# Performance work log

Hardware: AMD Instinct MI355X
Metric: run time of the kernel (lower is better)

Reference implementation:

```python
import jax, jax.numpy as jnp
import numpy as np

N_F = 100000   # station (feature) nodes
N_H = 49152    # healpix nodes (12*4^6)
E = 400000     # edges per timestep
T_IN = 12
T_OUT = 12
H = 64         # hidden_size (must equal 64: cat with Linear(1,64) output)
A_H = 2 * H    # AttentionReadout hidden_size


def setup_inputs() -> dict:
    key = jax.random.key(0)
    ks = jax.random.split(key, 20)
    feat = jax.random.normal(ks[0], (N_F, T_IN, 1), dtype=jnp.float32)
    enc_src = jax.random.randint(ks[1], (E,), 0, N_F, dtype=jnp.int32)
    enc_dst = jax.random.randint(ks[2], (E,), 0, N_H, dtype=jnp.int32)
    dec_src = jax.random.randint(ks[3], (E,), 0, N_H, dtype=jnp.int32)
    dec_dst = jax.random.randint(ks[4], (E,), 0, N_F, dtype=jnp.int32)
    s = 0.05
    return {
        'feat': feat,
        'enc_src': enc_src, 'enc_dst': enc_dst,
        'dec_src': dec_src, 'dec_dst': dec_dst,
        # per-timestep encoder GraphConv(1 -> H) weights
        'W_enc': jax.random.normal(ks[5], (T_IN, 1, H), jnp.float32) * s,
        'b_enc': jnp.zeros((T_IN, H), jnp.float32),
        # MLP processor over time: Linear(T_IN -> T_OUT) + ReLU
        'W_proc': jax.random.normal(ks[6], (T_IN, T_OUT), jnp.float32) * s,
        'b_proc': jnp.zeros((T_OUT,), jnp.float32),
        # per-timestep decoder GraphConv(H -> H)
        'W_dec': jax.random.normal(ks[7], (T_OUT, H, H), jnp.float32) * s,
        'b_dec': jnp.zeros((T_OUT, H), jnp.float32),
        # decoder self.linears = Linear(1, 64)
        'W_lin': jax.random.normal(ks[8], (1, H), jnp.float32) * s,
        'b_lin': jnp.zeros((H,), jnp.float32),
        # AttentionReadout: score MLP (H -> 2H -> 1), output proj (H -> 1)
        'W_a1': jax.random.normal(ks[9], (H, A_H), jnp.float32) * s,
        'b_a1': jnp.zeros((A_H,), jnp.float32),
        'W_a2': jax.random.normal(ks[10], (A_H, 1), jnp.float32) * s,
        'b_a2': jnp.zeros((1,), jnp.float32),
        'W_o': jax.random.normal(ks[11], (H, 1), jnp.float32) * s,
        'b_o': jnp.zeros((1,), jnp.float32),
    }


def _gcn_norms(src, dst, n_src, n_dst):
    # DGL GraphConv norm='both': deg clamped to min 1, ^-0.5
    ones = jnp.ones(src.shape[0], jnp.float32)
    out_deg = jnp.maximum(jax.ops.segment_sum(ones, src, num_segments=n_src), 1.0)
    in_deg = jnp.maximum(jax.ops.segment_sum(ones, dst, num_segments=n_dst), 1.0)
    return out_deg ** -0.5, in_deg ** -0.5


def reference(feat, enc_src, enc_dst, dec_src, dec_dst,
              W_enc, b_enc, W_proc, b_proc, W_dec, b_dec,
              W_lin, b_lin, W_a1, b_a1, W_a2, b_a2, W_o, b_o):
    c_se, c_de = _gcn_norms(enc_src, enc_dst, N_F, N_H)
    c_sd, c_dd = _gcn_norms(dec_src, dec_dst, N_H, N_F)

    # ---- Graph_Encoder: per-t GraphConv(station -> healpix), 1 -> H ----
    x = jnp.nan_to_num(feat)                                  # [N_f, T_in, 1]
    msg = x * c_se[:, None, None]
    agg = jax.ops.segment_sum(msg[enc_src], enc_dst, num_segments=N_H)  # [N_h, T_in, 1]
    h_enc = jax.nn.leaky_relu(
        jnp.einsum('nti,tih->nth', agg * c_de[:, None, None], W_enc) + b_enc)  # [N_h, T_in, H]

    # ---- MLP_Processor: Linear over the time axis, T_in -> T_out, ReLU ----
    h_proc = jax.nn.relu(jnp.einsum('nth,to->noh', h_enc, W_proc)
                         + b_proc[:, None])                    # [N_h, T_out, H]
    h_proc_t = jnp.swapaxes(h_proc, 0, 1)                      # [T_out, N_h, H]

    # ---- Graph_Decoder: per-t GraphConv(healpix -> station) + Linear(prev) + AttentionReadout ----
    def step(y_prev, inp):
        h_t, W_t, b_t = inp                                    # h_t: [N_h, H]
        m = h_t * c_sd[:, None]
        a = jax.ops.segment_sum(m[dec_src], dec_dst, num_segments=N_F)  # [N_f, H]
        space1 = jax.nn.leaky_relu((a * c_dd[:, None]) @ W_t + b_t)     # [N_f, H]
        space2 = y_prev @ W_lin + b_lin                                 # [N_f, H]
        stacked = jnp.stack([space1, space2], axis=0)                   # [2, N_f, H]
        scores = jnp.tanh(stacked @ W_a1 + b_a1) @ W_a2 + b_a2          # [2, N_f, 1]
        alpha = jax.nn.softmax(scores, axis=0)
        states = jnp.sum(alpha * stacked, axis=0)                       # [N_f, H]
        y = states @ W_o + b_o                                          # [N_f, 1]
        return y, y

    y0 = x[:, -1]                                              # t{input_length-1}
    _, ys = jax.lax.scan(step, y0, (h_proc_t, W_dec, b_dec))
    return ys                                                  # [T_out, N_f, 1]
```

## Files before the change

kernel.cpp:

```cpp
#include <hip/hip_runtime.h>
#include <hip/hip_bf16.h>
#include <hip/hip_fp16.h>

#define NF 100000
#define NH 49152
#define EDG 400000
#define SLOTD 24
#define SLOTE 32

typedef __attribute__((ext_vector_type(8))) short short8;
typedef __attribute__((ext_vector_type(4))) float float4v;
typedef unsigned short u16;
typedef unsigned int u32;

__device__ __forceinline__ u16 f2b(float x) {
    u32 u = __float_as_uint(x);
    u32 r = u + 0x7FFFu + ((u >> 16) & 1u);
    return (u16)(r >> 16);
}
__device__ __forceinline__ u32 cvt_pk(float lo, float hi) {
    u32 r;
    asm("v_cvt_pk_bf16_f32 %0, %1, %2" : "=v"(r) : "v"(lo), "v"(hi));
    return r;
}
__device__ __forceinline__ __half2 h2(u32 v) { union { u32 u; __half2 h; } c; c.u = v; return c.h; }
__device__ __forceinline__ float fast_tanh(float x) {
    float t = __builtin_amdgcn_exp2f(x * 2.885390081777927f);
    return fmaf(-2.0f, __builtin_amdgcn_rcpf(t + 1.0f), 1.0f);
}

#define PN1 (NF * 12)
#define PN3 298304
#define PN4 384
#define PREB 5856
__global__ void init_all(u32* __restrict__ csrD32,
                         u32* __restrict__ degcnt, u32* __restrict__ mzero, int zstride,
                         const float* __restrict__ W_dec, const float* __restrict__ W_a1,
                         u16* __restrict__ fragWdec, u16* __restrict__ fragWa1,
                         const float* __restrict__ W_lin, const float* __restrict__ b_lin,
                         const float* __restrict__ b_a1, const float* __restrict__ W_o,
                         float* __restrict__ uvs, const float* __restrict__ W_a2,
                         float* __restrict__ gtab) {
    __shared__ float uvl[256];
    const int b = blockIdx.x;
    if (b < PREB) {
        int i = b * 256 + threadIdx.x;
        if (i < PN1) csrD32[i] = ((u32)NH << 16) | (u32)NH;
        else if (i < PN1 + PN3) degcnt[i - PN1] = 0u;
        else if (i < PN1 + PN3 + PN4) {
            int j = i - PN1 - PN3;
            mzero[(j >> 7) * (size_t)zstride + (j & 127)] = 0u;
        }
    } else if (b < PREB + 28) {
        int gid = (b - PREB) * 256 + threadIdx.x;
        if (gid >= 7168) return;
        int L = gid & 63;
        int f = gid >> 6;
        int q = L >> 4, cb = L & 15;
        if (f < 96) {
            int fr = f & 7;
            int c = fr >> 1, kc = fr & 1;
            int k0 = kc * 32 + q * 8;
            int nn = c * 16 + cb;
            int t = f >> 3;
            #pragma unroll
            for (int j = 0; j < 8; ++j)
                fragWdec[(f * 64 + L) * 8 + j] = f2b(W_dec[t * 4096 + (k0 + j) * 64 + nn]);
        } else {
            int fr = f - 96;
            int c2 = fr >> 1, kc = fr & 1;
            int k0 = kc * 32 + q * 8;
            int nn = c2 * 16 + cb;
            #pragma unroll
            for (int j = 0; j < 8; ++j)
                fragWa1[(fr * 64 + L) * 8 + j] = f2b(W_a1[(k0 + j) * 128 + nn]);
        }
    } else if (b == PREB + 28) {
        int k = threadIdx.x;
        if (k < 128) {
            float su = 0.f, sv = 0.f;
            for (int h = 0; h < 64; ++h) {
                su = fmaf(W_lin[h], W_a1[h * 128 + k], su);
                sv = fmaf(b_lin[h], W_a1[h * 128 + k], sv);
            }
            uvs[k] = su;
            uvs[128 + k] = sv + b_a1[k];
            if (k == 0) {
                float a = 0.f, bb = 0.f;
                for (int h = 0; h < 64; ++h) {
                    a = fmaf(W_lin[h], W_o[h], a);
                    bb = fmaf(b_lin[h], W_o[h], bb);
                }
                uvs[256] = a;
                uvs[257] = bb;
            }
        }
    } else {
        int k = threadIdx.x;
        if (k < 128) {
            float su = 0.f, sv = 0.f;
            for (int h = 0; h < 64; ++h) {
                su = fmaf(W_lin[h], W_a1[h * 128 + k], su);
                sv = fmaf(b_lin[h], W_a1[h * 128 + k], sv);
            }
            uvl[k] = su;
            uvl[128 + k] = sv + b_a1[k];
        }
        __syncthreads();
        int i = (b - PREB - 29) * 256 + threadIdx.x;
        if (i <= 16384) {
            float y = fmaf((float)i, 1.f / 256.f, -32.f);
            float s = 0.f;
            for (int kk = 0; kk < 128; ++kk)
                s = fmaf(fast_tanh(fmaf(y, uvl[kk], uvl[128 + kk])), W_a2[kk], s);
            gtab[i] = s;
        }
    }
}

__global__ void fill_slotted(const int* __restrict__ enc_src, const int* __restrict__ enc_dst,
                             const int* __restrict__ dec_src, const int* __restrict__ dec_dst,
                             int* __restrict__ cntD, u16* __restrict__ csrD, float* __restrict__ deg_sd,
                             int* __restrict__ cntE, u32* __restrict__ csrE, float* __restrict__ deg_se) {
    int e = blockIdx.x * 256 + threadIdx.x;
    if (e >= EDG) return;
    int ds = dec_src[e], dd = dec_dst[e];
    int i1 = atomicAdd(&cntD[dd], 1);
    if (i1 < SLOTD) csrD[(size_t)dd * SLOTD + i1] = (u16)ds;
    atomicAdd(&deg_sd[ds], 1.0f);
    int es = enc_src[e], ed = enc_dst[e];
    int i2 = atomicAdd(&cntE[ed], 1);
    if (i2 < SLOTE) csrE[(size_t)ed * SLOTE + i2] = (u32)es;
    atomicAdd(&deg_se[es], 1.0f);
}

__global__ __launch_bounds__(256) void enc_make(
    const float* __restrict__ feat, const float* __restrict__ deg_se,
    const int* __restrict__ cntE, const u32* __restrict__ csrE,
    const float* __restrict__ deg_sd, const float* __restrict__ W_enc,
    const float* __restrict__ b_enc, const float* __restrict__ W_proc,
    const float* __restrict__ b_proc, u16* __restrict__ m, size_t cstride) {
    __shared__ __align__(16) float aggl[4][12];
    const int tid = threadIdx.x, lane = tid & 63, wid = tid >> 6;
    const int n = blockIdx.x * 4 + wid;
    const int q = lane >> 2, l = lane & 3;
    int cntRaw = cntE[n];
    int cnt = cntRaw > SLOTE ? SLOTE : cntRaw;
    const u32* cp = csrE + (size_t)n * SLOTE;
    float4 a = {0.f, 0.f, 0.f, 0.f};
    if (l < 3) {
        for (int e = q; e < cnt; e += 16) {
            u32 s = cp[e];
            float c = rsqrtf(fmaxf(deg_se[s], 1.0f));
            float4 w = *(const float4*)(feat + (size_t)s * 12 + l * 4);
            w.x = (w.x != w.x) ? 0.f : w.x; w.y = (w.y != w.y) ? 0.f : w.y;
            w.z = (w.z != w.z) ? 0.f : w.z; w.w = (w.w != w.w) ? 0.f : w.w;
            a.x = fmaf(w.x, c, a.x); a.y = fmaf(w.y, c, a.y);
            a.z = fmaf(w.z, c, a.z); a.w = fmaf(w.w, c, a.w);
        }
    }
    #pragma unroll
    for (int mm = 4; mm < 64; mm <<= 1) {
        a.x += __shfl_xor(a.x, mm); a.y += __shfl_xor(a.y, mm);
        a.z += __shfl_xor(a.z, mm); a.w += __shfl_xor(a.w, mm);
    }
    if (q == 0 && l < 3) *(float4*)(&aggl[wid][l * 4]) = a;
    asm volatile("s_waitcnt lgkmcnt(0)" ::: "memory");

    const int h = lane;
    float cde = rsqrtf(fmaxf((float)cntRaw, 1.0f));
    float csd = rsqrtf(fmaxf(deg_sd[n], 1.0f));
    float he[12];
    #pragma unroll
    for (int ti = 0; ti < 12; ++ti) {
        float av = aggl[wid][ti] * cde;
        float x = fmaf(av, W_enc[ti * 64 + h], b_enc[ti * 64 + h]);
        he[ti] = x > 0.f ? x : 0.01f * x;
    }
    #pragma unroll
    for (int c = 0; c < 3; ++c) {
        float s0v[4];
        #pragma unroll
        for (int tt = 0; tt < 4; ++tt) {
            int t = c * 4 + tt;
            float s = b_proc[t];
            #pragma unroll
            for (int ti = 0; ti < 12; ++ti) s = fmaf(he[ti], W_proc[ti * 12 + t], s);
            s0v[tt] = fmaxf(s, 0.f) * csd;
        }
        u16 r0 = __half_as_ushort(__float2half(s0v[0]));
        u16 r1 = __half_as_ushort(__float2half(s0v[1]));
        u16 r2 = __half_as_ushort(__float2half(s0v[2]));
        u16 r3 = __half_as_ushort(__float2half(s0v[3]));
        u32 o0 = ((u32)r1 << 16) | r0;
        u32 o1 = ((u32)r3 << 16) | r2;
        u32* dst = (u32*)(m + c * cstride + (size_t)n * 256 + h * 4);
        dst[0] = o0; dst[1] = o1;
    }
}

__global__ __launch_bounds__(256) void enc_gather(const float* __restrict__ feat,
                                                  const float* __restrict__ deg_se,
                                                  const int* __restrict__ cntE,
                                                  const u32* __restrict__ csrE,
                                                  float* __restrict__ agg) {
    const int tid = threadIdx.x, lane = tid & 63, wid = tid >> 6;
    const int grp = lane >> 2, l = lane & 3;
    const int dst = blockIdx.x * 64 + wid * 16 + grp;
    int cnt = cntE[dst];
    if (cnt > SLOTE) cnt = SLOTE;
    const u32* cp = csrE + (size_t)dst * SLOTE;
    float4 a = {0.f, 0.f, 0.f, 0.f};
    if (l < 3) {
        for (int e = 0; e < cnt; ++e) {
            u32 s = cp[e];
            float c = rsqrtf(fmaxf(deg_se[s], 1.0f));
            float4 w = *(const float4*)(feat + (size_t)s * 12 + l * 4);
            w.x = (w.x != w.x) ? 0.f : w.x; w.y = (w.y != w.y) ? 0.f : w.y;
            w.z = (w.z != w.z) ? 0.f : w.z; w.w = (w.w != w.w) ? 0.f : w.w;
            a.x = fmaf(w.x, c, a.x); a.y = fmaf(w.y, c, a.y);
            a.z = fmaf(w.z, c, a.z); a.w = fmaf(w.w, c, a.w);
        }
    }
    *(float4*)(agg + (size_t)dst * 16 + l * 4) = a;
}

__global__ void make_chunk(const float* __restrict__ agg, const int* __restrict__ cntE,
                           const float* __restrict__ deg_sd, const float* __restrict__ W_enc,
                           const float* __restrict__ b_enc, const float* __restrict__ W_proc,
                           const float* __restrict__ b_proc, u16* __restrict__ m, int t0) {
    int gid = blockIdx.x * 256 + threadIdx.x;
    if (gid >= NH * 64) return;
    int n = gid >> 6, h = gid & 63;
    float cde = rsqrtf(fmaxf((float)cntE[n], 1.0f));
    float csd = rsqrtf(fmaxf(deg_sd[n], 1.0f));
    float he[12];
    #pragma unroll
    for (int ti = 0; ti < 12; ++ti) {
        float a = agg[n * 16 + ti] * cde;
        float x = fmaf(a, W_enc[ti * 64 + h], b_enc[ti * 64 + h]);
        he[ti] = x > 0.f ? x : 0.01f * x;
    }
    u16 r[4];
    #pragma unroll
    for (int tt = 0; tt < 4; ++tt) {
        int t = t0 + tt;
        float s = b_proc[t];
        #pragma unroll
        for (int ti = 0; ti < 12; ++ti) s = fmaf(he[ti], W_proc[ti * 12 + t], s);
        s = fmaxf(s, 0.f) * csd;
        r[tt] = __half_as_ushort(__float2half(s));
    }
    u32 o0 = ((u32)r[1] << 16) | r[0];
    u32 o1 = ((u32)r[3] << 16) | r[2];
    u32* dst = (u32*)(m + (size_t)n * 256 + h * 4);
    dst[0] = o0; dst[1] = o1;
}

__device__ __forceinline__ void acc4(__half2* a8, const u16* mrow, u32 lo, u32 hi) {
    int s0 = (int)(lo & 0xFFFF), s1 = (int)(lo >> 16);
    int s2 = (int)(hi & 0xFFFF), s3 = (int)(hi >> 16);
    const uint4* r0 = (const uint4*)(mrow + (size_t)s0 * 256);
    const uint4* r1 = (const uint4*)(mrow + (size_t)s1 * 256);
    const uint4* r2 = (const uint4*)(mrow + (size_t)s2 * 256);
    const uint4* r3 = (const uint4*)(mrow + (size_t)s3 * 256);
    uint4 A0 = r0[0], B0 = r0[1];
    uint4 A1 = r1[0], B1 = r1[1];
    uint4 A2 = r2[0], B2 = r2[1];
    uint4 A3 = r3[0], B3 = r3[1];
    a8[0] = __hadd2(a8[0], __hadd2(__hadd2(h2(A0.x), h2(A1.x)), __hadd2(h2(A2.x), h2(A3.x))));
    a8[1] = __hadd2(a8[1], __hadd2(__hadd2(h2(A0.y), h2(A1.y)), __hadd2(h2(A2.y), h2(A3.y))));
    a8[2] = __hadd2(a8[2], __hadd2(__hadd2(h2(A0.z), h2(A1.z)), __hadd2(h2(A2.z), h2(A3.z))));
    a8[3] = __hadd2(a8[3], __hadd2(__hadd2(h2(A0.w), h2(A1.w)), __hadd2(h2(A2.w), h2(A3.w))));
    a8[4] = __hadd2(a8[4], __hadd2(__hadd2(h2(B0.x), h2(B1.x)), __hadd2(h2(B2.x), h2(B3.x))));
    a8[5] = __hadd2(a8[5], __hadd2(__hadd2(h2(B0.y), h2(B1.y)), __hadd2(h2(B2.y), h2(B3.y))));
    a8[6] = __hadd2(a8[6], __hadd2(__hadd2(h2(B0.z), h2(B1.z)), __hadd2(h2(B2.z), h2(B3.z))));
    a8[7] = __hadd2(a8[7], __hadd2(__hadd2(h2(B0.w), h2(B1.w)), __hadd2(h2(B2.w), h2(B3.w))));
}

__global__ __launch_bounds__(256, 4) void dec_batch(
    const u16* __restrict__ mbase, const int* __restrict__ cntD, const u16* __restrict__ csrD,
    const u16* __restrict__ fragWdec, const u16* __restrict__ fragWa1,
    const float* __restrict__ b_dec, const float* __restrict__ b_a1,
    const float* __restrict__ W_a2, const float* __restrict__ W_o,
    float* __restrict__ S1, float* __restrict__ PW, int t0p, size_t mstride) {
    __shared__ __align__(16) u16 zs[18432];

    const u16* m = mbase + (size_t)blockIdx.y * mstride;
    const int t0 = t0p + blockIdx.y * 4;
    const int tid = threadIdx.x, lane = tid & 63, wid = tid >> 6;
    const int nw = blockIdx.x * 64 + wid * 16;
    const int g16 = lane >> 4, c16 = lane & 15;
    u16* zw0 = zs + wid * 4608;

    int cdw[4]; float cdd[4]; int nnv[4];
    uint4 qa[4];
    #pragma unroll
    for (int k = 0; k < 4; ++k) {
        int n = nw + g16 * 4 + k;
        bool v = (n < NF);
        nnv[k] = v ? n : 0;
        int cd = cntD[nnv[k]];
        cdd[k] = v ? rsqrtf(fmaxf((float)cd, 1.0f)) : 0.f;
        cdw[k] = v ? (cd > SLOTD ? SLOTD : cd) : 0;
        qa[k] = *(const uint4*)(csrD + (size_t)nnv[k] * SLOTD);
    }
    int cdmax = max(max(cdw[0], cdw[1]), max(cdw[2], cdw[3]));

    __half2 acc[4][8];
    #pragma unroll
    for (int k = 0; k < 4; ++k)
        #pragma unroll
        for (int i = 0; i < 8; ++i)
            acc[k][i] = __half2{__half(0.f), __half(0.f)};

    const u16* mrow = m + c16 * 16;
    #pragma unroll
    for (int k = 0; k < 4; ++k) if (cdw[k] > 0) acc4(acc[k], mrow, qa[k].x, qa[k].y);
    #pragma unroll
    for (int k = 0; k < 4; ++k) if (cdw[k] > 4) acc4(acc[k], mrow, qa[k].z, qa[k].w);
    if (__any(cdmax > 8)) {
        #pragma unroll
        for (int k = 0; k < 4; ++k) if (cdw[k] > 8) qa[k] = *(const uint4*)(csrD + (size_t)nnv[k] * SLOTD + 8);
        #pragma unroll
        for (int k = 0; k < 4; ++k) if (cdw[k] > 8) acc4(acc[k], mrow, qa[k].x, qa[k].y);
        #pragma unroll
        for (int k = 0; k < 4; ++k) if (cdw[k] > 12) acc4(acc[k], mrow, qa[k].z, qa[k].w);
        if (__any(cdmax > 16)) {
            #pragma unroll
            for (int k = 0; k < 4; ++k) if (cdw[k] > 16) qa[k] = *(const uint4*)(csrD + (size_t)nnv[k] * SLOTD + 16);
            #pragma unroll
            for (int k = 0; k < 4; ++k) if (cdw[k] > 16) acc4(acc[k], mrow, qa[k].x, qa[k].y);
            #pragma unroll
            for (int k = 0; k < 4; ++k) if (cdw[k] > 20) acc4(acc[k], mrow, qa[k].z, qa[k].w);
        }
    }

    #pragma unroll
    for (int k = 0; k < 4; ++k) {
        int j = g16 * 4 + k;
        float s = cdd[k];
        #pragma unroll
        for (int p = 0; p < 2; ++p) {
            float2 c0 = __half22float2(acc[k][0 * 2 + p]);
            float2 c1 = __half22float2(acc[k][1 * 2 + p]);
            float2 c2 = __half22float2(acc[k][2 * 2 + p]);
            float2 c3 = __half22float2(acc[k][3 * 2 + p]);
            u32 oA0 = cvt_pk(c0.x * s, c1.x * s);
            u32 oA1 = cvt_pk(c2.x * s, c3.x * s);
            u32 oB0 = cvt_pk(c0.y * s, c1.y * s);
            u32 oB1 = cvt_pk(c2.y * s, c3.y * s);
            u32* dA = (u32*)(zw0 + (2 * p) * 1152 + j * 72 + c16 * 4);
            u32* dB = (u32*)(zw0 + (2 * p + 1) * 1152 + j * 72 + c16 * 4);
            dA[0] = oA0; dA[1] = oA1;
            dB[0] = oB0; dB[1] = oB1;
        }
    }
    asm volatile("s_waitcnt lgkmcnt(0)" ::: "memory");

    float baw[8], waw[8], wov[4];
    #pragma unroll
    for (int c8 = 0; c8 < 8; ++c8) {
        int k = c8 * 16 + c16;
        baw[c8] = b_a1[k];
        waw[c8] = W_a2[k];
    }
    #pragma unroll
    for (int cc = 0; cc < 4; ++cc) wov[cc] = W_o[cc * 16 + c16];

    for (int tt = 0; tt < 4; ++tt) {
        const int t = t0 + tt;
        u16* zw = zw0 + tt * 1152;
        const u16* ab = zw + c16 * 72 + g16 * 8;
        short8 a0 = *(const short8*)ab;
        short8 a1 = *(const short8*)(ab + 32);

        const u16* fw = fragWdec + (size_t)t * 4096;
        float4v C1[4];
        #pragma unroll
        for (int cc = 0; cc < 4; ++cc) {
            float4v z4 = {0.f, 0.f, 0.f, 0.f};
            short8 b0 = *(const short8*)(fw + (cc * 2 + 0) * 512 + lane * 8);
            short8 b1 = *(const short8*)(fw + (cc * 2 + 1) * 512 + lane * 8);
            z4 = __builtin_amdgcn_mfma_f32_16x16x32_bf16(a0, b0, z4, 0, 0, 0);
            C1[cc] = __builtin_amdgcn_mfma_f32_16x16x32_bf16(a1, b1, z4, 0, 0, 0);
        }

        float pw[4] = {0.f, 0.f, 0.f, 0.f};
        #pragma unroll
        for (int cc = 0; cc < 4; ++cc) {
            float bt = b_dec[t * 64 + cc * 16 + c16];
            float wo = wov[cc];
            #pragma unroll
            for (int r = 0; r < 4; ++r) {
                float xx = C1[cc][r] + bt;
                float sp = xx > 0.f ? xx : 0.01f * xx;
                pw[r] = fmaf(sp, wo, pw[r]);
                zw[(g16 * 4 + r) * 72 + cc * 16 + c16] = f2b(sp);
            }
        }
        asm volatile("s_waitcnt lgkmcnt(0)" ::: "memory");
        short8 sa0 = *(const short8*)ab;
        short8 sa1 = *(const short8*)(ab + 32);

        float p1[4] = {0.f, 0.f, 0.f, 0.f};
        #pragma unroll
        for (int half = 0; half < 2; ++half) {
            float4v C2[4];
            #pragma unroll
            for (int cc = 0; cc < 4; ++cc) {
                int c8 = half * 4 + cc;
                float4v z4 = {0.f, 0.f, 0.f, 0.f};
                short8 b0 = *(const short8*)(fragWa1 + (c8 * 2 + 0) * 512 + lane * 8);
                short8 b1 = *(const short8*)(fragWa1 + (c8 * 2 + 1) * 512 + lane * 8);
                z4 = __builtin_amdgcn_mfma_f32_16x16x32_bf16(sa0, b0, z4, 0, 0, 0);
                C2[cc] = __builtin_amdgcn_mfma_f32_16x16x32_bf16(sa1, b1, z4, 0, 0, 0);
            }
            #pragma unroll
            for (int cc = 0; cc < 4; ++cc) {
                int c8 = half * 4 + cc;
                float ba = baw[c8], wa = waw[c8];
                #pragma unroll
                for (int r = 0; r < 4; ++r)
                    p1[r] = fmaf(fast_tanh(C2[cc][r] + ba), wa, p1[r]);
            }
        }

        #pragma unroll
        for (int mm = 1; mm < 16; mm <<= 1) {
            #pragma unroll
            for (int r = 0; r < 4; ++r) {
                p1[r] += __shfl_xor(p1[r], mm);
                pw[r] += __shfl_xor(pw[r], mm);
            }
        }

        if (c16 == 0) {
            #pragma unroll
            for (int r = 0; r < 4; ++r) {
                int n = nw + g16 * 4 + r;
                if (n < NF) {
                    S1[(size_t)t * NF + n] = p1[r];
                    PW[(size_t)t * NF + n] = pw[r];
                }
            }
        }
    }
}

__global__ __launch_bounds__(256) void dec_scan(
    const float* __restrict__ S1, const float* __restrict__ PW,
    const float* __restrict__ gtab, const float* __restrict__ uvs,
    const float* __restrict__ feat, const float* __restrict__ b_a2p,
    const float* __restrict__ b_op, float* __restrict__ out) {
    const int n = blockIdx.x * 256 + threadIdx.x;
    if (n >= NF) return;
    float s1v[12], pwv[12];
    #pragma unroll
    for (int t = 0; t < 12; ++t) {
        s1v[t] = S1[(size_t)t * NF + n];
        pwv[t] = PW[(size_t)t * NF + n];
    }
    const float wlo = uvs[256], blo = uvs[257], ba2 = b_a2p[0], bo = b_op[0];
    float yp = feat[n * 12 + 11];
    yp = (yp != yp) ? 0.f : yp;
    #pragma unroll
    for (int t = 0; t < 12; ++t) {
        float xf = fminf(fmaxf(fmaf(yp, 256.f, 8192.f), 0.f), 16383.f);
        int idx = (int)xf;
        float fr = xf - (float)idx;
        float g0 = gtab[idx], g1 = gtab[idx + 1];
        float p2 = fmaf(g1 - g0, fr, g0);
        float s1s = s1v[t] + ba2, s2s = p2 + ba2;
        float mx = fmaxf(s1s, s2s);
        float e1 = __expf(s1s - mx), e2 = __expf(s2s - mx);
        float y = (e1 * pwv[t] + e2 * fmaf(wlo, yp, blo)) / (e1 + e2) + bo;
        out[(size_t)t * NF + n] = y;
        yp = y;
    }
}

extern "C" void kernel_launch(void* const* d_in, const int* in_sizes, int n_in,
                              void* d_out, int out_size, void* d_ws, size_t ws_size,
                              hipStream_t stream) {
    const float* feat   = (const float*)d_in[0];
    const int* enc_src  = (const int*)d_in[1];
    const int* enc_dst  = (const int*)d_in[2];
    const int* dec_src  = (const int*)d_in[3];
    const int* dec_dst  = (const int*)d_in[4];
    const float* W_enc  = (const float*)d_in[5];
    const float* b_enc  = (const float*)d_in[6];
    const float* W_proc = (const float*)d_in[7];
    const float* b_proc = (const float*)d_in[8];
    const float* W_dec  = (const float*)d_in[9];
    const float* b_dec  = (const float*)d_in[10];
    const float* W_lin  = (const float*)d_in[11];
    const float* b_lin  = (const float*)d_in[12];
    const float* W_a1   = (const float*)d_in[13];
    const float* b_a1   = (const float*)d_in[14];
    const float* W_a2   = (const float*)d_in[15];
    const float* b_a2   = (const float*)d_in[16];
    const float* W_o    = (const float*)d_in[17];
    const float* b_o    = (const float*)d_in[18];
    float* out = (float*)d_out;

    float* W = (float*)d_ws;
    float* deg_se   = W;
    float* deg_sd   = W + 100000;
    int*   cntD     = (int*)(W + 149152);
    int*   cntE     = (int*)(W + 249152);
    float* uvs      = W + 298304;
    u16*   fragWdec = (u16*)(W + 298624);
    u16*   fragWa1  = (u16*)(W + 323200);
    float* agg      = W + 327296;
    float* S1       = W + 1113728;
    float* PW       = W + 2313728;
    u16*   csrD     = (u16*)(W + 3513728);
    u32*   csrE     = (u32*)(W + 4713728);
    float* gtab     = W + 6286592;
    u16*   m_ws     = (u16*)(W + 6303104);

    const size_t CSTRIDE = (size_t)(NH + 1) * 256;
    const size_t need_full = ((size_t)6303104 + 3 * CSTRIDE / 2) * 4;
    const bool full = ws_size >= need_full;
    const int zstride = full ? (int)(CSTRIDE / 2) : 0;

    init_all<<<PREB + 29 + 65, 256, 0, stream>>>((u32*)csrD, (u32*)W,
                                                 (u32*)m_ws + (size_t)NH * 128, zstride,
                                                 W_dec, W_a1, fragWdec, fragWa1,
                                                 W_lin, b_lin, b_a1, W_o, uvs, W_a2, gtab);
    fill_slotted<<<(EDG + 255) / 256, 256, 0, stream>>>(enc_src, enc_dst, dec_src, dec_dst,
                                                        cntD, csrD, deg_sd, cntE, csrE, deg_se);

    const int dec_grid = (NF + 63) / 64;
    if (full) {
        enc_make<<<NH / 4, 256, 0, stream>>>(feat, deg_se, cntE, csrE, deg_sd,
                                             W_enc, b_enc, W_proc, b_proc, m_ws, CSTRIDE);
        for (int c = 0; c < 3; ++c) {
            dec_batch<<<dim3(dec_grid, 1), 256, 0, stream>>>(m_ws + (size_t)c * CSTRIDE,
                                                             cntD, csrD, fragWdec, fragWa1,
                                                             b_dec, b_a1, W_a2, W_o, S1, PW,
                                                             4 * c, 0);
        }
    } else {
        enc_gather<<<NH / 64, 256, 0, stream>>>(feat, deg_se, cntE, csrE, agg);
        for (int c = 0; c < 3; ++c) {
            make_chunk<<<(NH * 64) / 256, 256, 0, stream>>>(agg, cntE, deg_sd, W_enc, b_enc,
                                                            W_proc, b_proc, m_ws, 4 * c);
            dec_batch<<<dim3(dec_grid, 1), 256, 0, stream>>>(m_ws, cntD, csrD, fragWdec, fragWa1,
                                                             b_dec, b_a1, W_a2, W_o, S1, PW,
                                                             4 * c, 0);
        }
    }
    dec_scan<<<(NF + 255) / 256, 256, 0, stream>>>(S1, PW, gtab, uvs, feat, b_a2, b_o, out);
}
```

Baseline: 381.4 us.

## Shift healpix rows by one, memset-based init, vectorized edge fill, single batched decoder launch

```diff
diff --git a/kernel.cpp b/kernel.cpp
--- a/kernel.cpp
+++ b/kernel.cpp
@@ -29,30 +29,16 @@
     return fmaf(-2.0f, __builtin_amdgcn_rcpf(t + 1.0f), 1.0f);
 }
 
-#define PN1 (NF * 12)
-#define PN3 298304
-#define PN4 384
-#define PREB 5856
-__global__ void init_all(u32* __restrict__ csrD32,
-                         u32* __restrict__ degcnt, u32* __restrict__ mzero, int zstride,
-                         const float* __restrict__ W_dec, const float* __restrict__ W_a1,
-                         u16* __restrict__ fragWdec, u16* __restrict__ fragWa1,
-                         const float* __restrict__ W_lin, const float* __restrict__ b_lin,
-                         const float* __restrict__ b_a1, const float* __restrict__ W_o,
-                         float* __restrict__ uvs, const float* __restrict__ W_a2,
-                         float* __restrict__ gtab) {
+__global__ void init_small(const float* __restrict__ W_dec, const float* __restrict__ W_a1,
+                           u16* __restrict__ fragWdec, u16* __restrict__ fragWa1,
+                           const float* __restrict__ W_lin, const float* __restrict__ b_lin,
+                           const float* __restrict__ b_a1, const float* __restrict__ W_o,
+                           float* __restrict__ uvs, const float* __restrict__ W_a2,
+                           float* __restrict__ gtab) {
     __shared__ float uvl[256];
     const int b = blockIdx.x;
-    if (b < PREB) {
-        int i = b * 256 + threadIdx.x;
-        if (i < PN1) csrD32[i] = ((u32)NH << 16) | (u32)NH;
-        else if (i < PN1 + PN3) degcnt[i - PN1] = 0u;
-        else if (i < PN1 + PN3 + PN4) {
-            int j = i - PN1 - PN3;
-            mzero[(j >> 7) * (size_t)zstride + (j & 127)] = 0u;
-        }
-    } else if (b < PREB + 28) {
-        int gid = (b - PREB) * 256 + threadIdx.x;
+    if (b < 28) {
+        int gid = b * 256 + threadIdx.x;
         if (gid >= 7168) return;
         int L = gid & 63;
         int f = gid >> 6;
@@ -75,7 +61,7 @@
             for (int j = 0; j < 8; ++j)
                 fragWa1[(fr * 64 + L) * 8 + j] = f2b(W_a1[(k0 + j) * 128 + nn]);
         }
-    } else if (b == PREB + 28) {
+    } else if (b == 28) {
         int k = threadIdx.x;
         if (k < 128) {
             float su = 0.f, sv = 0.f;
@@ -107,7 +93,7 @@
             uvl[128 + k] = sv + b_a1[k];
         }
         __syncthreads();
-        int i = (b - PREB - 29) * 256 + threadIdx.x;
+        int i = (b - 29) * 256 + threadIdx.x;
         if (i <= 16384) {
             float y = fmaf((float)i, 1.f / 256.f, -32.f);
             float s = 0.f;
@@ -122,16 +108,31 @@
                              const int* __restrict__ dec_src, const int* __restrict__ dec_dst,
                              int* __restrict__ cntD, u16* __restrict__ csrD, float* __restrict__ deg_sd,
                              int* __restrict__ cntE, u32* __restrict__ csrE, float* __restrict__ deg_se) {
-    int e = blockIdx.x * 256 + threadIdx.x;
-    if (e >= EDG) return;
-    int ds = dec_src[e], dd = dec_dst[e];
-    int i1 = atomicAdd(&cntD[dd], 1);
-    if (i1 < SLOTD) csrD[(size_t)dd * SLOTD + i1] = (u16)ds;
-    atomicAdd(&deg_sd[ds], 1.0f);
-    int es = enc_src[e], ed = enc_dst[e];
-    int i2 = atomicAdd(&cntE[ed], 1);
-    if (i2 < SLOTE) csrE[(size_t)ed * SLOTE + i2] = (u32)es;
-    atomicAdd(&deg_se[es], 1.0f);
+    int e4 = (blockIdx.x * 256 + threadIdx.x) * 4;
+    if (e4 >= EDG) return;
+    int4 dsv = *(const int4*)(dec_src + e4);
+    int4 ddv = *(const int4*)(dec_dst + e4);
+    int4 esv = *(const int4*)(enc_src + e4);
+    int4 edv = *(const int4*)(enc_dst + e4);
+    int ds[4] = {dsv.x, dsv.y, dsv.z, dsv.w};
+    int dd[4] = {ddv.x, ddv.y, ddv.z, ddv.w};
+    int es[4] = {esv.x, esv.y, esv.z, esv.w};
+    int ed[4] = {edv.x, edv.y, edv.z, edv.w};
+    int i1[4], i2[4];
+    #pragma unroll
+    for (int j = 0; j < 4; ++j) i1[j] = atomicAdd(&cntD[dd[j]], 1);
+    #pragma unroll
+    for (int j = 0; j < 4; ++j) i2[j] = atomicAdd(&cntE[ed[j]], 1);
+    #pragma unroll
+    for (int j = 0; j < 4; ++j) atomicAdd(&deg_sd[ds[j]], 1.0f);
+    #pragma unroll
+    for (int j = 0; j < 4; ++j) atomicAdd(&deg_se[es[j]], 1.0f);
+    #pragma unroll
+    for (int j = 0; j < 4; ++j)
+        if (i1[j] < SLOTD) csrD[(size_t)dd[j] * SLOTD + i1[j]] = (u16)(ds[j] + 1);
+    #pragma unroll
+    for (int j = 0; j < 4; ++j)
+        if (i2[j] < SLOTE) csrE[(size_t)ed[j] * SLOTE + i2[j]] = (u32)es[j];
 }
 
 __global__ __launch_bounds__(256) void enc_make(
@@ -194,7 +195,7 @@
         u16 r3 = __half_as_ushort(__float2half(s0v[3]));
         u32 o0 = ((u32)r1 << 16) | r0;
         u32 o1 = ((u32)r3 << 16) | r2;
-        u32* dst = (u32*)(m + c * cstride + (size_t)n * 256 + h * 4);
+        u32* dst = (u32*)(m + c * cstride + (size_t)(n + 1) * 256 + h * 4);
         dst[0] = o0; dst[1] = o1;
     }
 }
@@ -253,7 +254,7 @@
     }
     u32 o0 = ((u32)r[1] << 16) | r[0];
     u32 o1 = ((u32)r[3] << 16) | r[2];
-    u32* dst = (u32*)(m + (size_t)n * 256 + h * 4);
+    u32* dst = (u32*)(m + (size_t)(n + 1) * 256 + h * 4);
     dst[0] = o0; dst[1] = o1;
 }
 
@@ -523,25 +524,28 @@
     const size_t CSTRIDE = (size_t)(NH + 1) * 256;
     const size_t need_full = ((size_t)6303104 + 3 * CSTRIDE / 2) * 4;
     const bool full = ws_size >= need_full;
-    const int zstride = full ? (int)(CSTRIDE / 2) : 0;
-
-    init_all<<<PREB + 29 + 65, 256, 0, stream>>>((u32*)csrD, (u32*)W,
-                                                 (u32*)m_ws + (size_t)NH * 128, zstride,
-                                                 W_dec, W_a1, fragWdec, fragWa1,
-                                                 W_lin, b_lin, b_a1, W_o, uvs, W_a2, gtab);
-    fill_slotted<<<(EDG + 255) / 256, 256, 0, stream>>>(enc_src, enc_dst, dec_src, dec_dst,
-                                                        cntD, csrD, deg_sd, cntE, csrE, deg_se);
+
+    hipMemsetAsync((void*)csrD, 0, (size_t)NF * SLOTD * 2, stream);
+    hipMemsetAsync((void*)W, 0, (size_t)298304 * 4, stream);
+    if (full) {
+        for (int c = 0; c < 3; ++c)
+            hipMemsetAsync((void*)(m_ws + (size_t)c * CSTRIDE), 0, 512, stream);
+    } else {
+        hipMemsetAsync((void*)m_ws, 0, 512, stream);
+    }
+
+    init_small<<<94, 256, 0, stream>>>(W_dec, W_a1, fragWdec, fragWa1,
+                                       W_lin, b_lin, b_a1, W_o, uvs, W_a2, gtab);
+    fill_slotted<<<(EDG / 4 + 255) / 256, 256, 0, stream>>>(enc_src, enc_dst, dec_src, dec_dst,
+                                                            cntD, csrD, deg_sd, cntE, csrE, deg_se);
 
     const int dec_grid = (NF + 63) / 64;
     if (full) {
         enc_make<<<NH / 4, 256, 0, stream>>>(feat, deg_se, cntE, csrE, deg_sd,
                                              W_enc, b_enc, W_proc, b_proc, m_ws, CSTRIDE);
-        for (int c = 0; c < 3; ++c) {
-            dec_batch<<<dim3(dec_grid, 1), 256, 0, stream>>>(m_ws + (size_t)c * CSTRIDE,
-                                                             cntD, csrD, fragWdec, fragWa1,
-                                                             b_dec, b_a1, W_a2, W_o, S1, PW,
-                                                             4 * c, 0);
-        }
+        dec_batch<<<dim3(dec_grid, 3), 256, 0, stream>>>(m_ws, cntD, csrD, fragWdec, fragWa1,
+                                                         b_dec, b_a1, W_a2, W_o, S1, PW,
+                                                         0, CSTRIDE);
     } else {
         enc_gather<<<NH / 64, 256, 0, stream>>>(feat, deg_se, cntE, csrE, agg);
         for (int c = 0; c < 3; ++c) {
```

After: 352.0 us. -7.7%, faster.

## Fuse CSR fill phases into encoder kernels and batch decoder chunks in one launch

Applied to the files above, without the earlier changes.

```diff
diff --git a/kernel.cpp b/kernel.cpp
--- a/kernel.cpp
+++ b/kernel.cpp
@@ -7,6 +7,7 @@
 #define EDG 400000
 #define SLOTD 24
 #define SLOTE 32
+#define FILLB 1563
 
 typedef __attribute__((ext_vector_type(8))) short short8;
 typedef __attribute__((ext_vector_type(4))) float float4v;
@@ -29,30 +30,32 @@
     return fmaf(-2.0f, __builtin_amdgcn_rcpf(t + 1.0f), 1.0f);
 }
 
-#define PN1 (NF * 12)
-#define PN3 298304
-#define PN4 384
-#define PREB 5856
-__global__ void init_all(u32* __restrict__ csrD32,
-                         u32* __restrict__ degcnt, u32* __restrict__ mzero, int zstride,
-                         const float* __restrict__ W_dec, const float* __restrict__ W_a1,
-                         u16* __restrict__ fragWdec, u16* __restrict__ fragWa1,
-                         const float* __restrict__ W_lin, const float* __restrict__ b_lin,
-                         const float* __restrict__ b_a1, const float* __restrict__ W_o,
-                         float* __restrict__ uvs, const float* __restrict__ W_a2,
-                         float* __restrict__ gtab) {
+__global__ __launch_bounds__(256) void init_fill_enc(
+    const int* __restrict__ enc_src, const int* __restrict__ enc_dst,
+    const int* __restrict__ dec_src,
+    int* __restrict__ cntE, u32* __restrict__ csrE,
+    float* __restrict__ deg_se, float* __restrict__ deg_sd,
+    const float* __restrict__ W_dec, const float* __restrict__ W_a1,
+    u16* __restrict__ fragWdec, u16* __restrict__ fragWa1,
+    const float* __restrict__ W_lin, const float* __restrict__ b_lin,
+    const float* __restrict__ b_a1, const float* __restrict__ W_o,
+    float* __restrict__ uvs, const float* __restrict__ W_a2,
+    float* __restrict__ gtab) {
     __shared__ float uvl[256];
     const int b = blockIdx.x;
-    if (b < PREB) {
-        int i = b * 256 + threadIdx.x;
-        if (i < PN1) csrD32[i] = ((u32)NH << 16) | (u32)NH;
-        else if (i < PN1 + PN3) degcnt[i - PN1] = 0u;
-        else if (i < PN1 + PN3 + PN4) {
-            int j = i - PN1 - PN3;
-            mzero[(j >> 7) * (size_t)zstride + (j & 127)] = 0u;
-        }
-    } else if (b < PREB + 28) {
-        int gid = (b - PREB) * 256 + threadIdx.x;
+    if (b < FILLB) {
+        int e = b * 256 + threadIdx.x;
+        if (e >= EDG) return;
+        int es = enc_src[e], ed = enc_dst[e], ds = dec_src[e];
+        int i2 = atomicAdd(&cntE[ed], 1);
+        atomicAdd(&deg_se[es], 1.0f);
+        atomicAdd(&deg_sd[ds], 1.0f);
+        if (i2 < SLOTE) csrE[(size_t)ed * SLOTE + i2] = (u32)es;
+        return;
+    }
+    const int b2 = b - FILLB;
+    if (b2 < 28) {
+        int gid = b2 * 256 + threadIdx.x;
         if (gid >= 7168) return;
         int L = gid & 63;
         int f = gid >> 6;
@@ -75,7 +78,7 @@
             for (int j = 0; j < 8; ++j)
                 fragWa1[(fr * 64 + L) * 8 + j] = f2b(W_a1[(k0 + j) * 128 + nn]);
         }
-    } else if (b == PREB + 28) {
+    } else if (b2 == 28) {
         int k = threadIdx.x;
         if (k < 128) {
             float su = 0.f, sv = 0.f;
@@ -107,7 +110,7 @@
             uvl[128 + k] = sv + b_a1[k];
         }
         __syncthreads();
-        int i = (b - PREB - 29) * 256 + threadIdx.x;
+        int i = (b2 - 29) * 256 + threadIdx.x;
         if (i <= 16384) {
             float y = fmaf((float)i, 1.f / 256.f, -32.f);
             float s = 0.f;
@@ -118,31 +121,35 @@
     }
 }
 
-__global__ void fill_slotted(const int* __restrict__ enc_src, const int* __restrict__ enc_dst,
-                             const int* __restrict__ dec_src, const int* __restrict__ dec_dst,
-                             int* __restrict__ cntD, u16* __restrict__ csrD, float* __restrict__ deg_sd,
-                             int* __restrict__ cntE, u32* __restrict__ csrE, float* __restrict__ deg_se) {
+__global__ void fill_dec(const int* __restrict__ dec_src, const int* __restrict__ dec_dst,
+                         int* __restrict__ cntD, u16* __restrict__ csrD) {
     int e = blockIdx.x * 256 + threadIdx.x;
     if (e >= EDG) return;
     int ds = dec_src[e], dd = dec_dst[e];
     int i1 = atomicAdd(&cntD[dd], 1);
-    if (i1 < SLOTD) csrD[(size_t)dd * SLOTD + i1] = (u16)ds;
-    atomicAdd(&deg_sd[ds], 1.0f);
-    int es = enc_src[e], ed = enc_dst[e];
-    int i2 = atomicAdd(&cntE[ed], 1);
-    if (i2 < SLOTE) csrE[(size_t)ed * SLOTE + i2] = (u32)es;
-    atomicAdd(&deg_se[es], 1.0f);
-}
-
-__global__ __launch_bounds__(256) void enc_make(
+    if (i1 < SLOTD) csrD[(size_t)dd * SLOTD + i1] = (u16)(ds + 1);
+}
+
+__global__ __launch_bounds__(256) void enc_make_fill_dec(
+    const int* __restrict__ dec_src, const int* __restrict__ dec_dst,
+    int* __restrict__ cntD, u16* __restrict__ csrD,
     const float* __restrict__ feat, const float* __restrict__ deg_se,
     const int* __restrict__ cntE, const u32* __restrict__ csrE,
     const float* __restrict__ deg_sd, const float* __restrict__ W_enc,
     const float* __restrict__ b_enc, const float* __restrict__ W_proc,
     const float* __restrict__ b_proc, u16* __restrict__ m, size_t cstride) {
     __shared__ __align__(16) float aggl[4][12];
+    const int b = blockIdx.x;
+    if (b < FILLB) {
+        int e = b * 256 + threadIdx.x;
+        if (e >= EDG) return;
+        int ds = dec_src[e], dd = dec_dst[e];
+        int i1 = atomicAdd(&cntD[dd], 1);
+        if (i1 < SLOTD) csrD[(size_t)dd * SLOTD + i1] = (u16)(ds + 1);
+        return;
+    }
     const int tid = threadIdx.x, lane = tid & 63, wid = tid >> 6;
-    const int n = blockIdx.x * 4 + wid;
+    const int n = (b - FILLB) * 4 + wid;
     const int q = lane >> 2, l = lane & 3;
     int cntRaw = cntE[n];
     int cnt = cntRaw > SLOTE ? SLOTE : cntRaw;
@@ -194,7 +201,7 @@
         u16 r3 = __half_as_ushort(__float2half(s0v[3]));
         u32 o0 = ((u32)r1 << 16) | r0;
         u32 o1 = ((u32)r3 << 16) | r2;
-        u32* dst = (u32*)(m + c * cstride + (size_t)n * 256 + h * 4);
+        u32* dst = (u32*)(m + c * cstride + (size_t)(n + 1) * 256 + h * 4);
         dst[0] = o0; dst[1] = o1;
     }
 }
@@ -253,7 +260,7 @@
     }
     u32 o0 = ((u32)r[1] << 16) | r[0];
     u32 o1 = ((u32)r[3] << 16) | r[2];
-    u32* dst = (u32*)(m + (size_t)n * 256 + h * 4);
+    u32* dst = (u32*)(m + (size_t)(n + 1) * 256 + h * 4);
     dst[0] = o0; dst[1] = o1;
 }
 
@@ -523,26 +530,32 @@
     const size_t CSTRIDE = (size_t)(NH + 1) * 256;
     const size_t need_full = ((size_t)6303104 + 3 * CSTRIDE / 2) * 4;
     const bool full = ws_size >= need_full;
-    const int zstride = full ? (int)(CSTRIDE / 2) : 0;
-
-    init_all<<<PREB + 29 + 65, 256, 0, stream>>>((u32*)csrD, (u32*)W,
-                                                 (u32*)m_ws + (size_t)NH * 128, zstride,
-                                                 W_dec, W_a1, fragWdec, fragWa1,
-                                                 W_lin, b_lin, b_a1, W_o, uvs, W_a2, gtab);
-    fill_slotted<<<(EDG + 255) / 256, 256, 0, stream>>>(enc_src, enc_dst, dec_src, dec_dst,
-                                                        cntD, csrD, deg_sd, cntE, csrE, deg_se);
+
+    hipMemsetAsync((void*)csrD, 0, (size_t)NF * SLOTD * 2, stream);
+    hipMemsetAsync((void*)W, 0, (size_t)298304 * 4, stream);
+    if (full) {
+        for (int c = 0; c < 3; ++c)
+            hipMemsetAsync((void*)(m_ws + (size_t)c * CSTRIDE), 0, 512, stream);
+    } else {
+        hipMemsetAsync((void*)m_ws, 0, 512, stream);
+    }
+
+    init_fill_enc<<<FILLB + 94, 256, 0, stream>>>(enc_src, enc_dst, dec_src,
+                                                  cntE, csrE, deg_se, deg_sd,
+                                                  W_dec, W_a1, fragWdec, fragWa1,
+                                                  W_lin, b_lin, b_a1, W_o, uvs, W_a2, gtab);
 
     const int dec_grid = (NF + 63) / 64;
     if (full) {
-        enc_make<<<NH / 4, 256, 0, stream>>>(feat, deg_se, cntE, csrE, deg_sd,
-                                             W_enc, b_enc, W_proc, b_proc, m_ws, CSTRIDE);
-        for (int c = 0; c < 3; ++c) {
-            dec_batch<<<dim3(dec_grid, 1), 256, 0, stream>>>(m_ws + (size_t)c * CSTRIDE,
-                                                             cntD, csrD, fragWdec, fragWa1,
-                                                             b_dec, b_a1, W_a2, W_o, S1, PW,
-                                                             4 * c, 0);
-        }
+        enc_make_fill_dec<<<FILLB + NH / 4, 256, 0, stream>>>(dec_src, dec_dst, cntD, csrD,
+                                                              feat, deg_se, cntE, csrE, deg_sd,
+                                                              W_enc, b_enc, W_proc, b_proc,
+                                                              m_ws, CSTRIDE);
+        dec_batch<<<dim3(dec_grid, 3), 256, 0, stream>>>(m_ws, cntD, csrD, fragWdec, fragWa1,
+                                                         b_dec, b_a1, W_a2, W_o, S1, PW,
+                                                         0, CSTRIDE);
     } else {
+        fill_dec<<<FILLB, 256, 0, stream>>>(dec_src, dec_dst, cntD, csrD);
         enc_gather<<<NH / 64, 256, 0, stream>>>(feat, deg_se, cntE, csrE, agg);
         for (int c = 0; c < 3; ++c) {
             make_chunk<<<(NH * 64) / 256, 256, 0, stream>>>(agg, cntE, deg_sd, W_enc, b_enc,
```

Result: faster. 351.3 us (-7.9%).
